# Kernel optimization log

Hardware: AMD Instinct MI355X
Metric: run time of the kernel (lower is better)

Reference implementation:

```python
import jax, jax.numpy as jnp
import numpy as np

H = 2048       # hidden_size
I = 5504       # intermediate_size
E = 8          # num_experts
TOPK = 2       # num_experts_per_tok


def setup_inputs() -> dict:
    key = jax.random.key(0)
    ks = jax.random.split(key, 5)
    s = 0.02
    x = jax.random.normal(ks[0], (2, 2048, H), dtype=jnp.float32)
    router_w = jax.random.normal(ks[1], (E, H), dtype=jnp.float32) * s   # Linear weight [out,in]
    Wg = jax.random.normal(ks[2], (E, I, H), dtype=jnp.float32) * s      # gate_proj per expert
    Wu = jax.random.normal(ks[3], (E, I, H), dtype=jnp.float32) * s      # up_proj per expert
    Wd = jax.random.normal(ks[4], (E, H, I), dtype=jnp.float32) * s      # down_proj per expert
    return {"x": x, "router_w": router_w, "Wg": Wg, "Wu": Wu, "Wd": Wd}


def reference(x, router_w, Wg, Wu, Wd):
    B, S, Hh = x.shape
    xf = x.reshape(-1, Hh)                                  # [T, H]
    logits = xf @ router_w.T                                # [T, E]
    top_vals, top_idx = jax.lax.top_k(logits, TOPK)         # [T, K]
    top_w = jax.nn.softmax(top_vals, axis=-1)               # softmax over selected logits only
    # combine weight per (token, expert): zero if expert not selected
    combine = jnp.sum(jax.nn.one_hot(top_idx, E, dtype=xf.dtype) * top_w[..., None], axis=1)  # [T, E]

    out = jnp.zeros_like(xf)
    for e in range(E):  # fixed small expert loop (unrolled under jit)
        h = jax.nn.silu(xf @ Wg[e].T) * (xf @ Wu[e].T)      # [T, I]
        y = h @ Wd[e].T                                     # [T, H]
        out = out + combine[:, e:e + 1] * y
    return out.reshape(B, S, Hh)
```

## Files before the change

kernel.cpp:

```cpp
#include <hip/hip_runtime.h>
#include <cstdint>
#include <cstddef>

#define HDIM 2048
#define IDIM 5504
#define NEXP 8
#define NTOK 4096
#define NROWS (2 * NTOK)

#define S1_NCT 43
#define S1_NRT 8
#define S1_NWG (S1_NCT * S1_NRT * NEXP)
#define S1_NK  (HDIM / 64)
#define S2_NCT 8
#define S2_NRT 8
#define S2_NWG (S2_NCT * S2_NRT * NEXP)
#define S2_NK  (IDIM / 64)

typedef _Float16 half8 __attribute__((ext_vector_type(8)));
typedef _Float16 half4v __attribute__((ext_vector_type(4)));
typedef float floatx4 __attribute__((ext_vector_type(4)));

#define GLOAD16(g, l)                                                         \
  __builtin_amdgcn_global_load_lds(                                           \
      (const __attribute__((address_space(1))) void*)(g),                     \
      (__attribute__((address_space(3))) void*)(l), 16, 0, 0)

#define SBAR()  asm volatile("s_barrier" ::: "memory")
#define VMCNT(n) asm volatile("s_waitcnt vmcnt(" #n ")" ::: "memory")

#define XH_OFF   0
#define HB_OFF   (XH_OFF + (size_t)NTOK * HDIM * 2)
#define BTOK_OFF (HB_OFF + (size_t)NROWS * IDIM * 2)
#define BW_OFF   (BTOK_OFF + 32768)
#define TOKP_OFF (BW_OFF + 32768)
#define TOKW_OFF (TOKP_OFF + 16384)
#define T2R_OFF  (TOKW_OFF + 32768)
#define META_OFF (T2R_OFF + 32768)
#define Y2_OFF   (META_OFF + 128)
#define WS_NEED_Y2 (Y2_OFF + (size_t)NROWS * HDIM * 2)
#define WG16_OFF (WS_NEED_Y2)
#define WU16_OFF (WG16_OFF + (size_t)NEXP * IDIM * HDIM * 2)
#define WD16_OFF (WU16_OFF + (size_t)NEXP * IDIM * HDIM * 2)


__global__ void cvt_x_kernel(const float4* __restrict__ x, half4v* __restrict__ xh, int n4) {
  int i = blockIdx.x * blockDim.x + threadIdx.x;
  int st = gridDim.x * blockDim.x;
  for (; i < n4; i += st) {
    float4 v = x[i];
    half4v o = { (_Float16)v.x, (_Float16)v.y, (_Float16)v.z, (_Float16)v.w };
    xh[i] = o;
  }
}

__global__ void cvt_w_kernel(const float4* __restrict__ w, half8* __restrict__ o, int n8) {
  int i = blockIdx.x * blockDim.x + threadIdx.x;
  int st = gridDim.x * blockDim.x;
  for (; i < n8; i += st) {
    float4 a = w[2 * i], b = w[2 * i + 1];
    o[i] = half8{ (_Float16)a.x, (_Float16)a.y, (_Float16)a.z, (_Float16)a.w,
                  (_Float16)b.x, (_Float16)b.y, (_Float16)b.z, (_Float16)b.w };
  }
}

__global__ void router_kernel(const float* __restrict__ x, const float* __restrict__ rw,
                              int* __restrict__ tokp, float2* __restrict__ tokw,
                              int* __restrict__ cnt) {
  int t = blockIdx.x * 4 + (threadIdx.x >> 6);
  int lane = threadIdx.x & 63;
  const float4* xr = (const float4*)(x + (size_t)t * HDIM);
  float acc[NEXP];
#pragma unroll
  for (int e = 0; e < NEXP; ++e) acc[e] = 0.f;
#pragma unroll
  for (int it = 0; it < HDIM / 256; ++it) {
    float4 xv = xr[lane + 64 * it];
#pragma unroll
    for (int e = 0; e < NEXP; ++e) {
      float4 wv = ((const float4*)(rw + (size_t)e * HDIM))[lane + 64 * it];
      acc[e] += xv.x * wv.x + xv.y * wv.y + xv.z * wv.z + xv.w * wv.w;
    }
  }
#pragma unroll
  for (int off = 32; off > 0; off >>= 1) {
#pragma unroll
    for (int e = 0; e < NEXP; ++e) acc[e] += __shfl_xor(acc[e], off);
  }
  if (lane == 0) {
    int e0 = 0; float v0 = acc[0];
#pragma unroll
    for (int e = 1; e < NEXP; ++e) {
      if (acc[e] > v0) { v0 = acc[e]; e0 = e; }
    }
    int e1 = -1; float v1 = -3.0e38f;
#pragma unroll
    for (int e = 0; e < NEXP; ++e) {
      if (e == e0) continue;
      if (acc[e] > v1) { v1 = acc[e]; e1 = e; }
    }
    float w0 = 1.f / (1.f + __expf(v1 - v0));
    tokp[t] = e0 | (e1 << 8);
    tokw[t] = make_float2(w0, 1.f - w0);
    atomicAdd(&cnt[e0], 1);
    atomicAdd(&cnt[e1], 1);
  }
}

__global__ void scan_kernel(const int* __restrict__ cnt, int* __restrict__ offp) {
  if (threadIdx.x == 0) {
    int s = 0;
    for (int e = 0; e < NEXP; ++e) { offp[e] = s; s += cnt[e]; }
    offp[NEXP] = s;
  }
}

__global__ void scatter_kernel(const int* __restrict__ tokp, const float2* __restrict__ tokw,
                               const int* __restrict__ offp, int* __restrict__ cursor,
                               int* __restrict__ btok, float* __restrict__ bw,
                               int* __restrict__ t2r) {
  int t = blockIdx.x * blockDim.x + threadIdx.x;
  if (t >= NTOK) return;
  int p = tokp[t];
  float2 w = tokw[t];
  int e0 = p & 0xff, e1 = (p >> 8) & 0xff;
  int r0 = offp[e0] + atomicAdd(&cursor[e0], 1);
  btok[r0] = t; bw[r0] = w.x; t2r[2 * t] = r0;
  int r1 = offp[e1] + atomicAdd(&cursor[e1], 1);
  btok[r1] = t; bw[r1] = w.y; t2r[2 * t + 1] = r1;
}

__global__ void combine_kernel(const _Float16* __restrict__ y2, const int* __restrict__ t2r,
                               const float2* __restrict__ tokw, float* __restrict__ out) {
  int idx = blockIdx.x * 256 + threadIdx.x;
  int t = idx >> 9, c = (idx & 511) * 4;
  int r0 = t2r[2 * t], r1 = t2r[2 * t + 1];
  float2 w = tokw[t];
  half4v v0 = *(const half4v*)(y2 + (size_t)r0 * HDIM + c);
  half4v v1 = *(const half4v*)(y2 + (size_t)r1 * HDIM + c);
  float4 o;
  o.x = w.x * (float)v0[0] + w.y * (float)v1[0];
  o.y = w.x * (float)v0[1] + w.y * (float)v1[1];
  o.z = w.x * (float)v0[2] + w.y * (float)v1[2];
  o.w = w.x * (float)v0[3] + w.y * (float)v1[3];
  *(float4*)(out + (size_t)t * HDIM + c) = o;
}

#define MFMA_Q(Q, BF)                                                          \
  {                                                                            \
    __builtin_amdgcn_s_setprio(1);                                             \
    _Pragma("unroll") for (int mi = 0; mi < 4; ++mi)                           \
      _Pragma("unroll") for (int ni = 0; ni < 2; ++ni)                         \
        _Pragma("unroll") for (int kk = 0; kk < 2; ++kk)                       \
          acc[Q][mi][ni] = __builtin_amdgcn_mfma_f32_16x16x32_f16(             \
              af[mi][kk], BF[ni][kk], acc[Q][mi][ni], 0, 0, 0);                \
    __builtin_amdgcn_s_setprio(0);                                             \
  }

__global__ __launch_bounds__(512, 2) void stage1_kernel(
    const _Float16* __restrict__ xh, const _Float16* __restrict__ Wg16,
    const int* __restrict__ offp, const int* __restrict__ btok, _Float16* __restrict__ hb) {
  int bid = blockIdx.x;
  int wg = (bid & 7) * (S1_NWG / 8) + (bid >> 3);
  int rt = wg % S1_NRT;
  int ct = (wg / S1_NRT) % S1_NCT;
  int e  = wg / (S1_NRT * S1_NCT);
  int base = offp[e];
  int ne = offp[e + 1] - base;
  if (rt * 256 >= ne) return;
  int valid = ne - rt * 256; if (valid > 256) valid = 256;
  int tid = threadIdx.x, lane = tid & 63, wave = tid >> 6;
  int qr = wave >> 2, qc = wave & 3;
  int lrow = lane & 15, kg = lane >> 4;

  __shared__ __attribute__((aligned(16))) _Float16 Ah[4][128 * 64];
  __shared__ __attribute__((aligned(16))) _Float16 Bh[4][128 * 64];

  const char* abase = (const char*)xh;
  const char* bbase = (const char*)(Wg16 + (size_t)e * IDIM * HDIM);

  uint32_t aoffB[2][2], boffB[2][2];
#pragma unroll
  for (int half = 0; half < 2; ++half) {
#pragma unroll
    for (int i = 0; i < 2; ++i) {
      int L = i * 512 + tid;
      int r = L >> 3, c = (L & 7) ^ (r & 7);
      int rl = half * 128 + r;
      int rr = (rl < valid) ? rl : (valid - 1);
      aoffB[half][i] = (uint32_t)(((uint32_t)btok[base + rt * 256 + rr] * HDIM + c * 8) * 2);
      size_t off = ((size_t)ct * 128 + r) * HDIM + (size_t)c * 8;
      if (half) off += (size_t)NEXP * IDIM * HDIM;
      boffB[half][i] = (uint32_t)(off * 2);
    }
  }
  int dst0 = wave * 1024;
  int dst1 = 8192 + wave * 1024;

  int aro[4][2], bro[2][2];
#pragma unroll
  for (int mi = 0; mi < 4; ++mi) {
    int r = qr * 64 + mi * 16 + lrow;
#pragma unroll
    for (int kk = 0; kk < 2; ++kk)
      aro[mi][kk] = (r * 8 + ((kk * 4 + kg) ^ (r & 7))) * 8;
  }
#pragma unroll
  for (int ni = 0; ni < 2; ++ni) {
    int r = qc * 32 + ni * 16 + lrow;
#pragma unroll
    for (int kk = 0; kk < 2; ++kk)
      bro[ni][kk] = (r * 8 + ((kk * 4 + kg) ^ (r & 7))) * 8;
  }

  floatx4 acc[4][4][2] = {};
  half8 af[4][2], b0f[2][2], b1f[2][2];

  auto STA = [&](int t, int half, _Float16* slot) {
    uint32_t kb = (uint32_t)((t < S1_NK) ? t : (S1_NK - 1)) * 128u;
    GLOAD16(abase + (aoffB[half][0] + kb), (char*)slot + dst0);
    GLOAD16(abase + (aoffB[half][1] + kb), (char*)slot + dst1);
  };
  auto STB = [&](int t, int half, _Float16* slot) {
    uint32_t kb = (uint32_t)((t < S1_NK) ? t : (S1_NK - 1)) * 128u;
    GLOAD16(bbase + (boffB[half][0] + kb), (char*)slot + dst0);
    GLOAD16(bbase + (boffB[half][1] + kb), (char*)slot + dst1);
  };
  auto LDA = [&](const _Float16* slot) {
#pragma unroll
    for (int mi = 0; mi < 4; ++mi)
#pragma unroll
      for (int kk = 0; kk < 2; ++kk) af[mi][kk] = *(const half8*)&slot[aro[mi][kk]];
  };
  auto LDB0 = [&](const _Float16* slot) {
#pragma unroll
    for (int ni = 0; ni < 2; ++ni)
#pragma unroll
      for (int kk = 0; kk < 2; ++kk) b0f[ni][kk] = *(const half8*)&slot[bro[ni][kk]];
  };
  auto LDB1 = [&](const _Float16* slot) {
#pragma unroll
    for (int ni = 0; ni < 2; ++ni)
#pragma unroll
      for (int kk = 0; kk < 2; ++kk) b1f[ni][kk] = *(const half8*)&slot[bro[ni][kk]];
  };

  STB(0, 0, Bh[0]); STA(0, 0, Ah[0]); STA(0, 1, Ah[1]); STB(0, 1, Bh[1]);

  for (int I = 0; I < S1_NK / 2; ++I) {
    int t1 = 2 * I + 1, t2 = 2 * I + 2;
    STB(t1, 0, Bh[2]);
    VMCNT(2);
    SBAR();
    LDA(Ah[0]); LDB0(Bh[0]);
    MFMA_Q(0, b0f);
    SBAR();
    STA(t1, 0, Ah[2]);
    SBAR();
    LDB1(Bh[1]);
    MFMA_Q(1, b1f);
    SBAR();
    STA(t1, 1, Ah[3]); STB(t1, 1, Bh[3]);
    SBAR();
    LDA(Ah[1]);
    MFMA_Q(2, b0f);
    SBAR();
    SBAR();
    MFMA_Q(3, b1f);
    SBAR();
    STB(t2, 0, Bh[0]);
    VMCNT(6);
    SBAR();
    LDA(Ah[2]); LDB0(Bh[2]);
    MFMA_Q(0, b0f);
    SBAR();
    STA(t2, 0, Ah[0]);
    VMCNT(4);
    SBAR();
    LDB1(Bh[3]);
    MFMA_Q(1, b1f);
    SBAR();
    STA(t2, 1, Ah[1]); STB(t2, 1, Bh[1]);
    SBAR();
    LDA(Ah[3]);
    MFMA_Q(2, b0f);
    SBAR();
    SBAR();
    MFMA_Q(3, b1f);
    SBAR();
  }

  size_t hrow_base = (size_t)(base + rt * 256);
#pragma unroll
  for (int qrow = 0; qrow < 2; ++qrow) {
#pragma unroll
    for (int mi = 0; mi < 4; ++mi) {
#pragma unroll
      for (int j = 0; j < 4; ++j) {
        int r = qrow * 128 + qr * 64 + mi * 16 + kg * 4 + j;
        if (r < valid) {
#pragma unroll
          for (int ni = 0; ni < 2; ++ni) {
            float g = acc[qrow * 2][mi][ni][j];
            float u = acc[qrow * 2 + 1][mi][ni][j];
            float hv = g / (1.f + __expf(-g)) * u;
            int cidx = ct * 128 + qc * 32 + ni * 16 + lrow;
            hb[(hrow_base + r) * IDIM + cidx] = (_Float16)hv;
          }
        }
      }
    }
  }
}

__global__ __launch_bounds__(512, 2) void stage2_kernel(
    const _Float16* __restrict__ hb, const _Float16* __restrict__ Wd16,
    const int* __restrict__ offp, _Float16* __restrict__ y2) {
  int bid = blockIdx.x;
  int wg = (bid & 7) * (S2_NWG / 8) + (bid >> 3);
  int rt = wg % S2_NRT;
  int ct = (wg / S2_NRT) % S2_NCT;
  int e  = wg / (S2_NRT * S2_NCT);
  int base = offp[e];
  int ne = offp[e + 1] - base;
  if (rt * 256 >= ne) return;
  int valid = ne - rt * 256; if (valid > 256) valid = 256;
  int tid = threadIdx.x, lane = tid & 63, wave = tid >> 6;
  int qr = wave >> 2, qc = wave & 3;
  int lrow = lane & 15, kg = lane >> 4;

  __shared__ __attribute__((aligned(16))) _Float16 Ah[4][128 * 64];
  __shared__ __attribute__((aligned(16))) _Float16 Bh[4][128 * 64];

  const char* abase = (const char*)hb;
  const char* bbase = (const char*)(Wd16 + (size_t)e * HDIM * IDIM);

  uint32_t aoffB[2][2], boffB[2][2];
#pragma unroll
  for (int half = 0; half < 2; ++half) {
#pragma unroll
    for (int i = 0; i < 2; ++i) {
      int L = i * 512 + tid;
      int r = L >> 3, c = (L & 7) ^ (r & 7);
      int rl = half * 128 + r;
      int rr = (rl < valid) ? rl : (valid - 1);
      aoffB[half][i] = (uint32_t)(((size_t)(base + rt * 256 + rr) * IDIM + (size_t)c * 8) * 2);
      boffB[half][i] = (uint32_t)((((size_t)ct * 256 + half * 128 + r) * IDIM + (size_t)c * 8) * 2);
    }
  }
  int dst0 = wave * 1024;
  int dst1 = 8192 + wave * 1024;

  int aro[4][2], bro[2][2];
#pragma unroll
  for (int mi = 0; mi < 4; ++mi) {
    int r = qr * 64 + mi * 16 + lrow;
#pragma unroll
    for (int kk = 0; kk < 2; ++kk)
      aro[mi][kk] = (r * 8 + ((kk * 4 + kg) ^ (r & 7))) * 8;
  }
#pragma unroll
  for (int ni = 0; ni < 2; ++ni) {
    int r = qc * 32 + ni * 16 + lrow;
#pragma unroll
    for (int kk = 0; kk < 2; ++kk)
      bro[ni][kk] = (r * 8 + ((kk * 4 + kg) ^ (r & 7))) * 8;
  }

  floatx4 acc[4][4][2] = {};
  half8 af[4][2], b0f[2][2], b1f[2][2];

  auto STA = [&](int t, int half, _Float16* slot) {
    uint32_t kb = (uint32_t)((t < S2_NK) ? t : (S2_NK - 1)) * 128u;
    GLOAD16(abase + (aoffB[half][0] + kb), (char*)slot + dst0);
    GLOAD16(abase + (aoffB[half][1] + kb), (char*)slot + dst1);
  };
  auto STB = [&](int t, int half, _Float16* slot) {
    uint32_t kb = (uint32_t)((t < S2_NK) ? t : (S2_NK - 1)) * 128u;
    GLOAD16(bbase + (boffB[half][0] + kb), (char*)slot + dst0);
    GLOAD16(bbase + (boffB[half][1] + kb), (char*)slot + dst1);
  };
  auto LDA = [&](const _Float16* slot) {
#pragma unroll
    for (int mi = 0; mi < 4; ++mi)
#pragma unroll
      for (int kk = 0; kk < 2; ++kk) af[mi][kk] = *(const half8*)&slot[aro[mi][kk]];
  };
  auto LDB0 = [&](const _Float16* slot) {
#pragma unroll
    for (int ni = 0; ni < 2; ++ni)
#pragma unroll
      for (int kk = 0; kk < 2; ++kk) b0f[ni][kk] = *(const half8*)&slot[bro[ni][kk]];
  };
  auto LDB1 = [&](const _Float16* slot) {
#pragma unroll
    for (int ni = 0; ni < 2; ++ni)
#pragma unroll
      for (int kk = 0; kk < 2; ++kk) b1f[ni][kk] = *(const half8*)&slot[bro[ni][kk]];
  };

  STB(0, 0, Bh[0]); STA(0, 0, Ah[0]); STA(0, 1, Ah[1]); STB(0, 1, Bh[1]);

  for (int I = 0; I < S2_NK / 2; ++I) {
    int t1 = 2 * I + 1, t2 = 2 * I + 2;
    STB(t1, 0, Bh[2]);
    VMCNT(2);
    SBAR();
    LDA(Ah[0]); LDB0(Bh[0]);
    MFMA_Q(0, b0f);
    SBAR();
    STA(t1, 0, Ah[2]);
    SBAR();
    LDB1(Bh[1]);
    MFMA_Q(1, b1f);
    SBAR();
    STA(t1, 1, Ah[3]); STB(t1, 1, Bh[3]);
    SBAR();
    LDA(Ah[1]);
    MFMA_Q(2, b0f);
    SBAR();
    SBAR();
    MFMA_Q(3, b1f);
    SBAR();
    STB(t2, 0, Bh[0]);
    VMCNT(6);
    SBAR();
    LDA(Ah[2]); LDB0(Bh[2]);
    MFMA_Q(0, b0f);
    SBAR();
    STA(t2, 0, Ah[0]);
    VMCNT(4);
    SBAR();
    LDB1(Bh[3]);
    MFMA_Q(1, b1f);
    SBAR();
    STA(t2, 1, Ah[1]); STB(t2, 1, Bh[1]);
    SBAR();
    LDA(Ah[3]);
    MFMA_Q(2, b0f);
    SBAR();
    SBAR();
    MFMA_Q(3, b1f);
    SBAR();
  }

#pragma unroll
  for (int qrow = 0; qrow < 2; ++qrow) {
#pragma unroll
    for (int mi = 0; mi < 4; ++mi) {
#pragma unroll
      for (int j = 0; j < 4; ++j) {
        int r = qrow * 128 + qr * 64 + mi * 16 + kg * 4 + j;
        if (r < valid) {
          size_t grow = (size_t)(base + rt * 256 + r);
#pragma unroll
          for (int qcol = 0; qcol < 2; ++qcol) {
#pragma unroll
            for (int ni = 0; ni < 2; ++ni) {
              int cidx = ct * 256 + qcol * 128 + qc * 32 + ni * 16 + lrow;
              y2[grow * HDIM + cidx] = (_Float16)acc[qrow * 2 + qcol][mi][ni][j];
            }
          }
        }
      }
    }
  }
}

extern "C" void kernel_launch(void* const* d_in, const int* in_sizes, int n_in,
                              void* d_out, int out_size, void* d_ws, size_t ws_size,
                              hipStream_t stream) {
  const float* x  = (const float*)d_in[0];
  const float* rw = (const float*)d_in[1];
  const float* Wg = (const float*)d_in[2];
  const float* Wu = (const float*)d_in[3];
  const float* Wd = (const float*)d_in[4];
  float* out = (float*)d_out;

  char* ws = (char*)d_ws;
  _Float16* xh  = (_Float16*)(ws + XH_OFF);
  _Float16* hb  = (_Float16*)(ws + HB_OFF);
  int*      btok = (int*)(ws + BTOK_OFF);
  float*    bwv  = (float*)(ws + BW_OFF);
  int*      tokp = (int*)(ws + TOKP_OFF);
  float2*   tokw = (float2*)(ws + TOKW_OFF);
  int*      t2r  = (int*)(ws + T2R_OFF);
  int*      meta = (int*)(ws + META_OFF);
  _Float16* y2   = (_Float16*)(ws + Y2_OFF);
  _Float16* wg16 = (_Float16*)(ws + WG16_OFF);
  _Float16* wu16 = (_Float16*)(ws + WU16_OFF);
  _Float16* wd16 = (_Float16*)(ws + WD16_OFF);
  int* cnt = meta;
  int* offp = meta + 8;
  int* cursor = meta + 20;

  hipMemsetAsync(meta, 0, 128, stream);

  cvt_x_kernel<<<2048, 256, 0, stream>>>((const float4*)x, (half4v*)xh, NTOK * HDIM / 4);
  router_kernel<<<NTOK / 4, 256, 0, stream>>>(x, rw, tokp, tokw, cnt);
  scan_kernel<<<1, 64, 0, stream>>>(cnt, offp);
  scatter_kernel<<<NTOK / 256, 256, 0, stream>>>(tokp, tokw, offp, cursor, btok, bwv, t2r);

  int n8 = NEXP * IDIM * HDIM / 8;
  cvt_w_kernel<<<2048, 256, 0, stream>>>((const float4*)Wg, (half8*)wg16, n8);
  cvt_w_kernel<<<2048, 256, 0, stream>>>((const float4*)Wu, (half8*)wu16, n8);
  cvt_w_kernel<<<2048, 256, 0, stream>>>((const float4*)Wd, (half8*)wd16, n8);

  stage1_kernel<<<S1_NWG, 512, 0, stream>>>(xh, wg16, offp, btok, hb);
  stage2_kernel<<<S2_NWG, 512, 0, stream>>>(hb, wd16, offp, y2);
  combine_kernel<<<NTOK * HDIM / 4 / 256, 256, 0, stream>>>(y2, t2r, tokw, out);
}
```

Baseline: 1.424 ms.

## Restructure GEMM main loop into uniform phases with deeper global-load prefetch

Replaces the hand-scheduled main loop in both GEMM stages with eight uniform phases. Each phase issues LDS fragment reads and one global-to-LDS stage, waits on lgkmcnt, runs one MFMA quadrant, and separates phases with barriers. The prologue now prefetches most of the next k-tile, so global loads run further ahead of compute and the number of barriers per iteration drops. The risk is that the tighter vmcnt accounting and buffer reuse could cause stalls or hazards if the load counts are off, and the loop may issue loads past the last k-tile.

```diff
diff --git a/kernel.cpp b/kernel.cpp
--- a/kernel.cpp
+++ b/kernel.cpp
@@ -26,8 +26,9 @@
       (const __attribute__((address_space(1))) void*)(g),                     \
       (__attribute__((address_space(3))) void*)(l), 16, 0, 0)
 
-#define SBAR()  asm volatile("s_barrier" ::: "memory")
+#define SBAR()   asm volatile("s_barrier" ::: "memory")
 #define VMCNT(n) asm volatile("s_waitcnt vmcnt(" #n ")" ::: "memory")
+#define LGKM0()  asm volatile("s_waitcnt lgkmcnt(0)" ::: "memory")
 
 #define XH_OFF   0
 #define HB_OFF   (XH_OFF + (size_t)NTOK * HDIM * 2)
@@ -155,6 +156,17 @@
           acc[Q][mi][ni] = __builtin_amdgcn_mfma_f32_16x16x32_f16(             \
               af[mi][kk], BF[ni][kk], acc[Q][mi][ni], 0, 0, 0);                \
     __builtin_amdgcn_s_setprio(0);                                             \
+  }
+
+#define PHASE(LDS_READS, STAGE1, VM, Q, BF)                                    \
+  {                                                                            \
+    LDS_READS;                                                                 \
+    STAGE1;                                                                    \
+    VM;                                                                        \
+    SBAR();                                                                    \
+    LGKM0();                                                                   \
+    MFMA_Q(Q, BF);                                                             \
+    SBAR();                                                                    \
   }
 
 __global__ __launch_bounds__(512, 2) void stage1_kernel(
@@ -245,49 +257,21 @@
       for (int kk = 0; kk < 2; ++kk) b1f[ni][kk] = *(const half8*)&slot[bro[ni][kk]];
   };
 
-  STB(0, 0, Bh[0]); STA(0, 0, Ah[0]); STA(0, 1, Ah[1]); STB(0, 1, Bh[1]);
+  STB(0, 0, Bh[0]); STA(0, 0, Ah[0]); STB(0, 1, Bh[1]); STA(0, 1, Ah[1]);
+  STB(1, 0, Bh[2]); STA(1, 0, Ah[2]); STB(1, 1, Bh[3]);
+  VMCNT(6);
+  SBAR();
 
   for (int I = 0; I < S1_NK / 2; ++I) {
-    int t1 = 2 * I + 1, t2 = 2 * I + 2;
-    STB(t1, 0, Bh[2]);
-    VMCNT(2);
-    SBAR();
-    LDA(Ah[0]); LDB0(Bh[0]);
-    MFMA_Q(0, b0f);
-    SBAR();
-    STA(t1, 0, Ah[2]);
-    SBAR();
-    LDB1(Bh[1]);
-    MFMA_Q(1, b1f);
-    SBAR();
-    STA(t1, 1, Ah[3]); STB(t1, 1, Bh[3]);
-    SBAR();
-    LDA(Ah[1]);
-    MFMA_Q(2, b0f);
-    SBAR();
-    SBAR();
-    MFMA_Q(3, b1f);
-    SBAR();
-    STB(t2, 0, Bh[0]);
-    VMCNT(6);
-    SBAR();
-    LDA(Ah[2]); LDB0(Bh[2]);
-    MFMA_Q(0, b0f);
-    SBAR();
-    STA(t2, 0, Ah[0]);
-    VMCNT(4);
-    SBAR();
-    LDB1(Bh[3]);
-    MFMA_Q(1, b1f);
-    SBAR();
-    STA(t2, 1, Ah[1]); STB(t2, 1, Bh[1]);
-    SBAR();
-    LDA(Ah[3]);
-    MFMA_Q(2, b0f);
-    SBAR();
-    SBAR();
-    MFMA_Q(3, b1f);
-    SBAR();
+    int t1 = 2 * I + 1, t0n = 2 * I + 2, t1n = 2 * I + 3;
+    PHASE(LDA(Ah[0]); LDB0(Bh[0]), STA(t1, 1, Ah[3]),            , 0, b0f);
+    PHASE(LDB1(Bh[1])            , STB(t0n, 0, Bh[0]),           , 1, b1f);
+    PHASE(LDA(Ah[1])             , STA(t0n, 0, Ah[0]),           , 2, b0f);
+    PHASE(                       , STB(t0n, 1, Bh[1]),  VMCNT(6) , 3, b1f);
+    PHASE(LDA(Ah[2]); LDB0(Bh[2]), STA(t0n, 1, Ah[1]),           , 0, b0f);
+    PHASE(LDB1(Bh[3])            , STB(t1n, 0, Bh[2]),           , 1, b1f);
+    PHASE(LDA(Ah[3])             , STA(t1n, 0, Ah[2]),           , 2, b0f);
+    PHASE(                       , STB(t1n, 1, Bh[3]),  VMCNT(6) , 3, b1f);
   }
 
   size_t hrow_base = (size_t)(base + rt * 256);
@@ -399,49 +383,21 @@
       for (int kk = 0; kk < 2; ++kk) b1f[ni][kk] = *(const half8*)&slot[bro[ni][kk]];
   };
 
-  STB(0, 0, Bh[0]); STA(0, 0, Ah[0]); STA(0, 1, Ah[1]); STB(0, 1, Bh[1]);
+  STB(0, 0, Bh[0]); STA(0, 0, Ah[0]); STB(0, 1, Bh[1]); STA(0, 1, Ah[1]);
+  STB(1, 0, Bh[2]); STA(1, 0, Ah[2]); STB(1, 1, Bh[3]);
+  VMCNT(6);
+  SBAR();
 
   for (int I = 0; I < S2_NK / 2; ++I) {
-    int t1 = 2 * I + 1, t2 = 2 * I + 2;
-    STB(t1, 0, Bh[2]);
-    VMCNT(2);
-    SBAR();
-    LDA(Ah[0]); LDB0(Bh[0]);
-    MFMA_Q(0, b0f);
-    SBAR();
-    STA(t1, 0, Ah[2]);
-    SBAR();
-    LDB1(Bh[1]);
-    MFMA_Q(1, b1f);
-    SBAR();
-    STA(t1, 1, Ah[3]); STB(t1, 1, Bh[3]);
-    SBAR();
-    LDA(Ah[1]);
-    MFMA_Q(2, b0f);
-    SBAR();
-    SBAR();
-    MFMA_Q(3, b1f);
-    SBAR();
-    STB(t2, 0, Bh[0]);
-    VMCNT(6);
-    SBAR();
-    LDA(Ah[2]); LDB0(Bh[2]);
-    MFMA_Q(0, b0f);
-    SBAR();
-    STA(t2, 0, Ah[0]);
-    VMCNT(4);
-    SBAR();
-    LDB1(Bh[3]);
-    MFMA_Q(1, b1f);
-    SBAR();
-    STA(t2, 1, Ah[1]); STB(t2, 1, Bh[1]);
-    SBAR();
-    LDA(Ah[3]);
-    MFMA_Q(2, b0f);
-    SBAR();
-    SBAR();
-    MFMA_Q(3, b1f);
-    SBAR();
+    int t1 = 2 * I + 1, t0n = 2 * I + 2, t1n = 2 * I + 3;
+    PHASE(LDA(Ah[0]); LDB0(Bh[0]), STA(t1, 1, Ah[3]),            , 0, b0f);
+    PHASE(LDB1(Bh[1])            , STB(t0n, 0, Bh[0]),           , 1, b1f);
+    PHASE(LDA(Ah[1])             , STA(t0n, 0, Ah[0]),           , 2, b0f);
+    PHASE(                       , STB(t0n, 1, Bh[1]),  VMCNT(6) , 3, b1f);
+    PHASE(LDA(Ah[2]); LDB0(Bh[2]), STA(t0n, 1, Ah[1]),           , 0, b0f);
+    PHASE(LDB1(Bh[3])            , STB(t1n, 0, Bh[2]),           , 1, b1f);
+    PHASE(LDA(Ah[3])             , STA(t1n, 0, Ah[2]),           , 2, b0f);
+    PHASE(                       , STB(t1n, 1, Bh[3]),  VMCNT(6) , 3, b1f);
   }
 
 #pragma unroll
```

Result: faster. 1.376 ms (-3.4%).
